# Kernel optimization log

Measured on AMD Instinct MI355X. Metric: run time of the kernel, lower is better.

Reference implementation:

```python
import jax, jax.numpy as jnp
import numpy as np
import math

GAIN = 6.0
FREQ = 1000.0
Q = 0.707
SAMPLE_RATE = 44100


def _peaking_coeffs():
    # torchaudio.functional.equalizer_biquad coefficients (peaking EQ)
    w0 = 2.0 * math.pi * FREQ / SAMPLE_RATE
    A = math.exp(GAIN / 40.0 * math.log(10.0))
    alpha = math.sin(w0) / (2.0 * Q)
    b0 = 1.0 + alpha * A
    b1 = -2.0 * math.cos(w0)
    b2 = 1.0 - alpha * A
    a0 = 1.0 + alpha / A
    a1 = -2.0 * math.cos(w0)
    a2 = 1.0 - alpha / A
    # normalize by a0 (lfilter semantics)
    return (np.float32(b0 / a0), np.float32(b1 / a0), np.float32(b2 / a0),
            np.float32(a1 / a0), np.float32(a2 / a0))


def setup_inputs() -> dict:
    key = jax.random.key(0)
    x = jax.random.normal(key, (8, 2, 1200000), dtype=jnp.float32)
    return {"x": x}


def _biquad(x):
    # x: [B, C, T]; direct-form-I biquad with zero initial conditions
    b0, b1, b2, a1, a2 = _peaking_coeffs()
    # FIR part, fully vectorized: f[n] = b0*x[n] + b1*x[n-1] + b2*x[n-2]
    xp = jnp.pad(x, ((0, 0), (0, 0), (2, 0)))
    f = b0 * xp[..., 2:] + b1 * xp[..., 1:-1] + b2 * xp[..., :-2]
    # IIR part via scan over time: y[n] = f[n] - a1*y[n-1] - a2*y[n-2]
    f_t = jnp.moveaxis(f, -1, 0)  # [T, B, C]
    y0 = jnp.zeros(x.shape[:-1], dtype=x.dtype)

    def step(carry, ft):
        y1, y2 = carry
        y = ft - a1 * y1 - a2 * y2
        return (y, y1), y

    _, ys = jax.lax.scan(step, (y0, y0), f_t)
    return jnp.moveaxis(ys, 0, -1)  # [B, C, T]


def reference(x):
    return _biquad(x)
```

## Files before the change

kernel.cpp:

```cpp
#include <hip/hip_runtime.h>
#include <math.h>


typedef float f32x4 __attribute__((ext_vector_type(4)));

#define T_LEN 1200000
#define NCH   16
#define L     32
#define NR    64
#define NWARM 4
#define OUT_ROWS (NR - NWARM)
#define OUT_PER_SEG (OUT_ROWS * L)
#define SEGS_PER_CH (T_LEN / OUT_PER_SEG)
#define NSEG (SEGS_PER_CH * NCH)
#define WPB 4
#define NBLOCKS 512
#define NWAVES (NBLOCKS * WPB)
#define RSTRIDE 36
#define WAVE_LDS (NR * RSTRIDE)

struct Params {
    float b0, b1, b2, a1, a2;
    float lnr, theta, inv_sinth;
    float C[6][4];
};

struct Seg { const float* xc; float* yc; int g0; };

__device__ __forceinline__ Seg mkseg(int s, const float* __restrict__ x,
                                     float* __restrict__ y)
{
    int ch = s / SEGS_PER_CH;
    int si = s - ch * SEGS_PER_CH;
    Seg g;
    g.xc = x + (size_t)ch * T_LEN;
    g.yc = y + (size_t)ch * T_LEN;
    g.g0 = si * OUT_PER_SEG - NWARM * L;
    return g;
}

__device__ __forceinline__ void load_seg(f32x4 r[8], const Seg& s, int lane)
{
    #pragma unroll
    for (int it = 0; it < 8; ++it) {
        int g = s.g0 + (it << 8) + (lane << 2);
        f32x4 v = {0.f, 0.f, 0.f, 0.f};
        if (g >= 0 && g < T_LEN) v = *(const f32x4*)(s.xc + g);
        r[it] = v;
    }
}

__device__ __forceinline__ void stage_seg(float* __restrict__ xs, const f32x4 r[8],
                                          int lane)
{
    const int row0 = lane >> 3, j = (lane & 7) << 2;
    #pragma unroll
    for (int it = 0; it < 8; ++it) {
        int row = (it << 3) + row0;
        *(f32x4*)&xs[row * RSTRIDE + j] = r[it];
    }
}

__device__ __forceinline__ void process_seg(float* __restrict__ xs,
                                            const Seg& s, int lane,
                                            const Params& P,
                                            const float c1r[4], const float c2r[4])
{
    const int base = lane * RSTRIDE;

    float x1 = 0.f, x2 = 0.f;
    if (lane > 0) {
        x1 = xs[base - RSTRIDE + 31];
        x2 = xs[base - RSTRIDE + 30];
    }
    asm volatile("" ::: "memory");

    float v1 = 0.f, v2 = 0.f;
    #pragma unroll
    for (int b = 0; b < 8; ++b) {
        f32x4 xv = *(const f32x4*)&xs[base + (b << 2)];
        f32x4 yv;
        #pragma unroll
        for (int k = 0; k < 4; ++k) {
            float xk = xv[k];
            float f  = fmaf(P.b0, xk, fmaf(P.b1, x1, P.b2 * x2));
            float t2 = fmaf(-P.a2, v2, f);
            float yk = fmaf(-P.a1, v1, t2);
            v2 = v1; v1 = yk;
            x2 = x1; x1 = xk;
            yv[k] = yk;
        }
        *(f32x4*)&xs[base + (b << 2)] = yv;
    }

    #pragma unroll
    for (int k = 0; k < 6; ++k) {
        int d = 1 << k;
        float p1 = __shfl_up(v1, d);
        float p2 = __shfl_up(v2, d);
        if (lane < d) { p1 = 0.f; p2 = 0.f; }
        float n1 = fmaf(P.C[k][0], p1, fmaf(P.C[k][1], p2, v1));
        float n2 = fmaf(P.C[k][2], p1, fmaf(P.C[k][3], p2, v2));
        v1 = n1; v2 = n2;
    }
    float e1 = __shfl_up(v1, 1);
    float e2 = __shfl_up(v2, 1);
    if (lane == 0) { e1 = 0.f; e2 = 0.f; }

    const int j0 = (lane << 2) & 31;
    #pragma unroll
    for (int it = 0; it < 8; ++it) {
        int vo = (it << 6) + lane;
        int row = NWARM + (it << 3) + (lane >> 3);
        row = row > 63 ? 63 : row;
        float al = __shfl(e1, row);
        float be = __shfl(e2, row);
        if (vo < OUT_PER_SEG / 4) {
            f32x4 yv = *(const f32x4*)&xs[row * RSTRIDE + j0];
            f32x4 o;
            #pragma unroll
            for (int k = 0; k < 4; ++k)
                o[k] = fmaf(al, c1r[k], fmaf(be, c2r[k], yv[k]));
            int q = (vo << 2) + NWARM * L;
            __builtin_nontemporal_store(o, (f32x4*)(s.yc + s.g0 + q));
        }
    }
}

#define MEMBAR asm volatile("" ::: "memory")

__global__ __launch_bounds__(256, 2) void eq_kernel(const float* __restrict__ x,
                                                    float* __restrict__ y, Params P)
{
    __shared__ __align__(16) float lds[WPB * WAVE_LDS];
    const int lane = threadIdx.x & 63;
    const int wid  = threadIdx.x >> 6;
    float* xs = lds + wid * WAVE_LDS;
    const int w = blockIdx.x * WPB + wid;

    float c1r[4], c2r[4];
    {
        const int t0 = (lane << 2) & 31;
        float ph[5];
        #pragma unroll
        for (int k = 0; k < 5; ++k) {
            int t = t0 - 1 + k;
            ph[k] = (t < 0) ? 0.f
                            : expf(t * P.lnr) * sinf((t + 1) * P.theta) * P.inv_sinth;
        }
        #pragma unroll
        for (int k = 0; k < 4; ++k) {
            c1r[k] = fmaf(-P.a1, ph[k + 1], -P.a2 * ph[k]);
            c2r[k] = -P.a2 * ph[k + 1];
        }
    }

    const Seg s0 = mkseg(w,              x, y);
    const Seg s1 = mkseg(w + NWAVES,     x, y);
    const Seg s2 = mkseg(w + 2 * NWAVES, x, y);
    const Seg s3 = mkseg(w + 3 * NWAVES, x, y);
    const bool has4 = (w + 4 * NWAVES) < NSEG;
    const Seg s4 = mkseg(has4 ? (w + 4 * NWAVES) : w, x, y);

    f32x4 ra[8], rb[8];
    load_seg(ra, s0, lane);
    load_seg(rb, s1, lane);

    stage_seg(xs, ra, lane); MEMBAR;
    process_seg(xs, s0, lane, P, c1r, c2r);
    load_seg(ra, s2, lane);

    stage_seg(xs, rb, lane); MEMBAR;
    process_seg(xs, s1, lane, P, c1r, c2r);
    load_seg(rb, s3, lane);

    stage_seg(xs, ra, lane); MEMBAR;
    process_seg(xs, s2, lane, P, c1r, c2r);
    if (has4) load_seg(ra, s4, lane);

    stage_seg(xs, rb, lane); MEMBAR;
    process_seg(xs, s3, lane, P, c1r, c2r);

    if (has4) {
        stage_seg(xs, ra, lane); MEMBAR;
        process_seg(xs, s4, lane, P, c1r, c2r);
    }
}

extern "C" void kernel_launch(void* const* d_in, const int* in_sizes, int n_in,
                              void* d_out, int out_size, void* d_ws, size_t ws_size,
                              hipStream_t stream) {
    const float* x = (const float*)d_in[0];
    float* y = (float*)d_out;

    double w0    = 2.0 * M_PI * 1000.0 / 44100.0;
    double A     = exp(6.0 / 40.0 * log(10.0));
    double al    = sin(w0) / (2.0 * 0.707);
    double b0 = 1.0 + al * A;
    double b1 = -2.0 * cos(w0);
    double b2 = 1.0 - al * A;
    double a0 = 1.0 + al / A;
    double a1 = -2.0 * cos(w0);
    double a2 = 1.0 - al / A;
    b0 /= a0; b1 /= a0; b2 /= a0; a1 /= a0; a2 /= a0;

    Params P;
    P.b0 = (float)b0; P.b1 = (float)b1; P.b2 = (float)b2;
    P.a1 = (float)a1; P.a2 = (float)a2;

    double r     = sqrt(a2);
    double theta = acos(-a1 / (2.0 * r));
    P.lnr = (float)log(r);
    P.theta = (float)theta;
    P.inv_sinth = (float)(1.0 / sin(theta));

    double m00 = -a1, m01 = -a2, m10 = 1.0, m11 = 0.0;
    for (int s = 0; s < 5; ++s) {
        double t00 = m00 * m00 + m01 * m10;
        double t01 = m00 * m01 + m01 * m11;
        double t10 = m10 * m00 + m11 * m10;
        double t11 = m10 * m01 + m11 * m11;
        m00 = t00; m01 = t01; m10 = t10; m11 = t11;
    }
    for (int k = 0; k < 6; ++k) {
        P.C[k][0] = (float)m00; P.C[k][1] = (float)m01;
        P.C[k][2] = (float)m10; P.C[k][3] = (float)m11;
        double t00 = m00 * m00 + m01 * m10;
        double t01 = m00 * m01 + m01 * m11;
        double t10 = m10 * m00 + m11 * m10;
        double t11 = m10 * m01 + m11 * m11;
        m00 = t00; m01 = t01; m10 = t10; m11 = t11;
    }

    eq_kernel<<<NBLOCKS, 256, 0, stream>>>(x, y, P);
}
```

Before: 29.98 us.

## Truncate cross-lane carry scan to four lanes and double block count

Replaces the six-step log-depth prefix scan of lane-boundary IIR states with a direct sum over only the previous four lanes, relying on the filter's impulse response decaying to negligible values beyond about 128 samples. Separately, it doubles the grid to 1024 blocks with a launch-bounds occupancy hint of 4 and cuts per-wave work from five segments to three. This reduces shuffle and FMA latency in the serial carry step and raises parallelism, at the cost of exactness for slowly decaying carries and a shallower per-wave load/compute pipeline.

```diff
diff --git a/kernel.cpp b/kernel.cpp
--- a/kernel.cpp
+++ b/kernel.cpp
@@ -14,7 +14,7 @@
 #define SEGS_PER_CH (T_LEN / OUT_PER_SEG)
 #define NSEG (SEGS_PER_CH * NCH)
 #define WPB 4
-#define NBLOCKS 512
+#define NBLOCKS 1024
 #define NWAVES (NBLOCKS * WPB)
 #define RSTRIDE 36
 #define WAVE_LDS (NR * RSTRIDE)
@@ -22,7 +22,7 @@
 struct Params {
     float b0, b1, b2, a1, a2;
     float lnr, theta, inv_sinth;
-    float C[6][4];
+    float C[3][4];
 };
 
 struct Seg { const float* xc; float* yc; int g0; };
@@ -93,19 +93,21 @@
         *(f32x4*)&xs[base + (b << 2)] = yv;
     }
 
-    #pragma unroll
-    for (int k = 0; k < 6; ++k) {
-        int d = 1 << k;
-        float p1 = __shfl_up(v1, d);
-        float p2 = __shfl_up(v2, d);
-        if (lane < d) { p1 = 0.f; p2 = 0.f; }
-        float n1 = fmaf(P.C[k][0], p1, fmaf(P.C[k][1], p2, v1));
-        float n2 = fmaf(P.C[k][2], p1, fmaf(P.C[k][3], p2, v2));
-        v1 = n1; v2 = n2;
-    }
-    float e1 = __shfl_up(v1, 1);
-    float e2 = __shfl_up(v2, 1);
-    if (lane == 0) { e1 = 0.f; e2 = 0.f; }
+    float q11 = __shfl_up(v1, 1), q21 = __shfl_up(v2, 1);
+    float q12 = __shfl_up(v1, 2), q22 = __shfl_up(v2, 2);
+    float q13 = __shfl_up(v1, 3), q23 = __shfl_up(v2, 3);
+    float q14 = __shfl_up(v1, 4), q24 = __shfl_up(v2, 4);
+    if (lane < 1) { q11 = 0.f; q21 = 0.f; }
+    if (lane < 2) { q12 = 0.f; q22 = 0.f; }
+    if (lane < 3) { q13 = 0.f; q23 = 0.f; }
+    if (lane < 4) { q14 = 0.f; q24 = 0.f; }
+    float e1 = q11, e2 = q21;
+    e1 = fmaf(P.C[0][0], q12, fmaf(P.C[0][1], q22, e1));
+    e2 = fmaf(P.C[0][2], q12, fmaf(P.C[0][3], q22, e2));
+    e1 = fmaf(P.C[1][0], q13, fmaf(P.C[1][1], q23, e1));
+    e2 = fmaf(P.C[1][2], q13, fmaf(P.C[1][3], q23, e2));
+    e1 = fmaf(P.C[2][0], q14, fmaf(P.C[2][1], q24, e1));
+    e2 = fmaf(P.C[2][2], q14, fmaf(P.C[2][3], q24, e2));
 
     const int j0 = (lane << 2) & 31;
     #pragma unroll
@@ -129,7 +131,7 @@
 
 #define MEMBAR asm volatile("" ::: "memory")
 
-__global__ __launch_bounds__(256, 2) void eq_kernel(const float* __restrict__ x,
+__global__ __launch_bounds__(256, 4) void eq_kernel(const float* __restrict__ x,
                                                     float* __restrict__ y, Params P)
 {
     __shared__ __align__(16) float lds[WPB * WAVE_LDS];
@@ -155,12 +157,10 @@
         }
     }
 
-    const Seg s0 = mkseg(w,              x, y);
-    const Seg s1 = mkseg(w + NWAVES,     x, y);
-    const Seg s2 = mkseg(w + 2 * NWAVES, x, y);
-    const Seg s3 = mkseg(w + 3 * NWAVES, x, y);
-    const bool has4 = (w + 4 * NWAVES) < NSEG;
-    const Seg s4 = mkseg(has4 ? (w + 4 * NWAVES) : w, x, y);
+    const Seg s0 = mkseg(w,          x, y);
+    const Seg s1 = mkseg(w + NWAVES, x, y);
+    const bool has2 = (w + 2 * NWAVES) < NSEG;
+    const Seg s2 = mkseg(has2 ? (w + 2 * NWAVES) : w, x, y);
 
     f32x4 ra[8], rb[8];
     load_seg(ra, s0, lane);
@@ -168,22 +168,14 @@
 
     stage_seg(xs, ra, lane); MEMBAR;
     process_seg(xs, s0, lane, P, c1r, c2r);
-    load_seg(ra, s2, lane);
+    if (has2) load_seg(ra, s2, lane);
 
     stage_seg(xs, rb, lane); MEMBAR;
     process_seg(xs, s1, lane, P, c1r, c2r);
-    load_seg(rb, s3, lane);
-
-    stage_seg(xs, ra, lane); MEMBAR;
-    process_seg(xs, s2, lane, P, c1r, c2r);
-    if (has4) load_seg(ra, s4, lane);
-
-    stage_seg(xs, rb, lane); MEMBAR;
-    process_seg(xs, s3, lane, P, c1r, c2r);
-
-    if (has4) {
+
+    if (has2) {
         stage_seg(xs, ra, lane); MEMBAR;
-        process_seg(xs, s4, lane, P, c1r, c2r);
+        process_seg(xs, s2, lane, P, c1r, c2r);
     }
 }
 
@@ -222,14 +214,15 @@
         double t11 = m10 * m01 + m11 * m11;
         m00 = t00; m01 = t01; m10 = t10; m11 = t11;
     }
-    for (int k = 0; k < 6; ++k) {
-        P.C[k][0] = (float)m00; P.C[k][1] = (float)m01;
-        P.C[k][2] = (float)m10; P.C[k][3] = (float)m11;
-        double t00 = m00 * m00 + m01 * m10;
-        double t01 = m00 * m01 + m01 * m11;
-        double t10 = m10 * m00 + m11 * m10;
-        double t11 = m10 * m01 + m11 * m11;
-        m00 = t00; m01 = t01; m10 = t10; m11 = t11;
+    double p00 = m00, p01 = m01, p10 = m10, p11 = m11;
+    for (int k = 0; k < 3; ++k) {
+        P.C[k][0] = (float)p00; P.C[k][1] = (float)p01;
+        P.C[k][2] = (float)p10; P.C[k][3] = (float)p11;
+        double t00 = p00 * m00 + p01 * m10;
+        double t01 = p00 * m01 + p01 * m11;
+        double t10 = p10 * m00 + p11 * m10;
+        double t11 = p10 * m01 + p11 * m11;
+        p00 = t00; p01 = t01; p10 = t10; p11 = t11;
     }
 
     eq_kernel<<<NBLOCKS, 256, 0, stream>>>(x, y, P);
```

Measured after the change: 29.82 us. About the same (-0.5%).
